# Performance work log

Measured on AMD Instinct MI355X. Metric: run time of the kernel, lower is better.

The kernel has to match this reference:

```python
import jax, jax.numpy as jnp
import numpy as np

T = 8192   # sequence length (= max_seq_len)
E = 1024   # embedding dim
D = 11     # hard-coded projection dim in source


def setup_inputs() -> dict:
    key = jax.random.key(0)
    ks = jax.random.split(key, 6)
    s_e = 1.0 / np.sqrt(E)
    s_d = 1.0 / np.sqrt(D)
    return {
        "x": jax.random.randint(ks[0], (T,), 0, 32000, dtype=jnp.int64),
        "x_embeddings": jax.random.normal(ks[1], (T, E), dtype=jnp.float32),
        "Wk": jax.random.normal(ks[2], (D, E), dtype=jnp.float32) * s_e,
        "bk": jnp.zeros((D,), dtype=jnp.float32),
        "Wq": jax.random.normal(ks[3], (D, E), dtype=jnp.float32) * s_e,
        "bq": jnp.zeros((D,), dtype=jnp.float32),
        "Wv": jax.random.normal(ks[4], (D, E), dtype=jnp.float32) * s_e,
        "bv": jnp.zeros((D,), dtype=jnp.float32),
        "Wf": jax.random.normal(ks[5], (E, D), dtype=jnp.float32) * s_d,
        "bf": jnp.zeros((E,), dtype=jnp.float32),
    }


def reference(x, x_embeddings, Wk, bk, Wq, bq, Wv, bv, Wf, bf):
    t = x.shape[0]  # static under jit
    k = x_embeddings @ Wk.T + bk            # [T, D]
    q = x_embeddings @ Wq.T + bq            # [T, D]
    v = x_embeddings @ Wv.T + bv            # [T, D]
    att = q @ k.T                           # [T, T]; NOTE: no 1/sqrt(D) scaling in source
    causal = jnp.tril(jnp.ones((t, t), dtype=bool))
    att = jnp.where(causal, att, -jnp.inf)
    att = jax.nn.softmax(att, axis=1)       # dim=1 as in source
    res = att @ v                           # [T, D]
    return res @ Wf.T + bf                  # [T, E]
```

## Files before the change

### kernel.cpp

```cpp
#include <hip/hip_runtime.h>

#define T_SEQ 8192
#define E_DIM 1024
#define QS 36
#define QNEC 4
#define QKC 64
#define QX4 16
#define QXST 17
#define QRB 64
#define AJC 64
#define ARB 256
#define KVW 24
#define NSLOT 128
#define TR 16

__device__ __forceinline__ float2 pkfma(float2 a, float2 b, float2 c) {
    return make_float2(fmaf(a.x, b.x, c.x), fmaf(a.y, b.y, c.y));
}
__device__ __forceinline__ float2 f2(float x, float y) { return make_float2(x, y); }


__global__ __launch_bounds__(256) void qkv_proj(
    const float* __restrict__ xe,
    const float* __restrict__ Wk, const float* __restrict__ bk,
    const float* __restrict__ Wq, const float* __restrict__ bq,
    const float* __restrict__ Wv, const float* __restrict__ bv,
    float* __restrict__ partQ) {
    const int row0 = blockIdx.x * QRB;
    const int ec = blockIdx.y;
    const int lane = threadIdx.x & 63;
    const int wg = threadIdx.x >> 6;

    __shared__ float4 xT[QRB * QXST];
    __shared__ float4 wT[36 * QX4];

    float2 acc[9];
#pragma unroll
    for (int k = 0; k < 9; ++k) acc[k] = f2(0.f, 0.f);

    for (int cc = 0; cc < 4; ++cc) {
        const int cb = ec * 256 + cc * QKC;
        if (cc) __syncthreads();

#pragma unroll
        for (int t = 0; t < 4; ++t) {
            int idx = threadIdx.x + t * 256;
            int r = idx >> 4, c4 = idx & 15;
            xT[r * QXST + c4] =
                *(const float4*)(xe + (size_t)(row0 + r) * E_DIM + cb + c4 * 4);
        }
        for (int idx = threadIdx.x; idx < 36 * QX4; idx += 256) {
            int r = idx >> 4, c4 = idx & 15;
            float4 v = make_float4(0.f, 0.f, 0.f, 0.f);
            if (r < 33) {
                const float* base = (r < 11) ? (Wk + (size_t)r * E_DIM)
                                  : (r < 22) ? (Wq + (size_t)(r - 11) * E_DIM)
                                             : (Wv + (size_t)(r - 22) * E_DIM);
                v = *(const float4*)(base + cb + c4 * 4);
            }
            wT[idx] = v;
        }
        __syncthreads();

        const float4* xr = xT + lane * QXST;
        const float4* wr = wT + wg * 9 * QX4;
#pragma unroll 4
        for (int c4 = 0; c4 < QX4; ++c4) {
            float4 xv = xr[c4];
#pragma unroll
            for (int k = 0; k < 9; ++k) {
                float4 wv = wr[k * QX4 + c4];
                acc[k] = pkfma(f2(xv.x, xv.y), f2(wv.x, wv.y), acc[k]);
                acc[k] = pkfma(f2(xv.z, xv.w), f2(wv.z, wv.w), acc[k]);
            }
        }
    }

    __syncthreads();
    float* res = (float*)xT;
#pragma unroll
    for (int k = 0; k < 9; ++k) {
        int o = wg * 9 + k;
        bool live = (o < 33);
        int c = (o < 11) ? o : (o < 22) ? o + 1 : (o < 33) ? o + 2
              : (o == 33) ? 11 : (o == 34) ? 23 : 35;
        float b = 0.f;
        if (ec == 0 && live)
            b = (o < 11) ? bk[o] : (o < 22) ? bq[o - 11] : bv[o - 22];
        res[lane * 36 + c] = live ? (acc[k].x + acc[k].y + b) : 0.f;
    }
    __syncthreads();

    float4* dst = (float4*)(partQ + ((size_t)ec * T_SEQ + row0) * QS);
    for (int idx = threadIdx.x; idx < QRB * 9; idx += 256) {
        int r = idx / 9, f = idx % 9;
        dst[idx] = *(const float4*)(res + r * 36 + f * 4);
    }
}

__global__ __launch_bounds__(256) void reduceQ(const float* __restrict__ partQ,
                                               float* __restrict__ qkvF) {
    const size_t idx = (size_t)blockIdx.x * 256 + threadIdx.x;
    const float4* p = (const float4*)partQ;
    const size_t cs = (size_t)T_SEQ * (QS / 4);
    float4 s = make_float4(0.f, 0.f, 0.f, 0.f);
#pragma unroll
    for (int c = 0; c < QNEC; ++c) {
        float4 a = p[idx + (size_t)c * cs];
        s.x += a.x; s.y += a.y; s.z += a.z; s.w += a.w;
    }
    ((float4*)qkvF)[idx] = s;
}

__global__ __launch_bounds__(128) void attn(const float* __restrict__ qkvF,
                                            float* __restrict__ part) {
    const int b = blockIdx.x;
    int rb = 0;
    while ((rb + 1) * (rb + 2) <= b) ++rb;
    const int p = b - rb * (rb + 1);
    const int lane = threadIdx.x & 63;
    const int wid = threadIdx.x >> 6;
    const int jc = 2 * p + wid;
    const int r0 = rb * ARB + lane * 4;
    const int j0 = jc * AJC;

    float2 q[4][6], o[4][6];
#pragma unroll
    for (int i = 0; i < 4; ++i) {
        const float* qp = qkvF + (size_t)(r0 + i) * QS + 12;
#pragma unroll
        for (int d = 0; d < 5; ++d) q[i][d] = f2(qp[2 * d], qp[2 * d + 1]);
        q[i][5] = f2(qp[10], 0.f);
#pragma unroll
        for (int d = 0; d < 6; ++d) o[i][d] = f2(0.f, 0.f);
    }

    __shared__ float kvs[2][AJC * KVW];
    float* kv = kvs[wid];

#pragma unroll
    for (int t = 0; t < 6; ++t) {
        int idx = lane + t * 64;
        int row = idx / 6, f = idx % 6;
        int srcOff = f * 4 + (f >= 3 ? 12 : 0);
        float4 v = *(const float4*)(qkvF + (size_t)(j0 + row) * QS + srcOff);
        *(float4*)(kv + row * KVW + f * 4) = v;
    }
    __syncthreads();

    for (int jj = 0; jj < AJC; ++jj) {
        const float* kp = kv + jj * KVW;
        const float4 kA = *(const float4*)(kp);
        const float4 kB = *(const float4*)(kp + 4);
        const float4 kC = *(const float4*)(kp + 8);
        const float4 vA = *(const float4*)(kp + 12);
        const float4 vB = *(const float4*)(kp + 16);
        const float4 vC = *(const float4*)(kp + 20);
        const float2 k01 = f2(kA.x, kA.y), k23 = f2(kA.z, kA.w);
        const float2 k45 = f2(kB.x, kB.y), k67 = f2(kB.z, kB.w);
        const float2 k89 = f2(kC.x, kC.y), kXp = f2(kC.z, kC.w);
        const int j = j0 + jj;

#pragma unroll
        for (int i = 0; i < 4; ++i) {
            float2 s = pkfma(q[i][0], k01, pkfma(q[i][1], k23, pkfma(q[i][2], k45,
                       pkfma(q[i][3], k67, pkfma(q[i][4], k89,
                       pkfma(q[i][5], kXp, f2(0.f, 0.f)))))));
            float pe = __expf(s.x + s.y);
            pe = (j <= r0 + i) ? pe : 0.f;
            float2 p2 = f2(pe, pe);
            o[i][0] = pkfma(p2, f2(vA.x, vA.y), o[i][0]);
            o[i][1] = pkfma(p2, f2(vA.z, vA.w), o[i][1]);
            o[i][2] = pkfma(p2, f2(vB.x, vB.y), o[i][2]);
            o[i][3] = pkfma(p2, f2(vB.z, vB.w), o[i][3]);
            o[i][4] = pkfma(p2, f2(vC.x, vC.y), o[i][4]);
            o[i][5] = pkfma(p2, f2(vC.z, 1.f),  o[i][5]);
        }
    }

    float* d0 = part + ((size_t)jc * T_SEQ + r0) * 12;
#pragma unroll
    for (int i = 0; i < 4; ++i) {
        float4 t;
        t.x = o[i][0].x; t.y = o[i][0].y; t.z = o[i][1].x; t.w = o[i][1].y;
        *(float4*)(d0 + i * 12 + 0) = t;
        t.x = o[i][2].x; t.y = o[i][2].y; t.z = o[i][3].x; t.w = o[i][3].y;
        *(float4*)(d0 + i * 12 + 4) = t;
        t.x = o[i][4].x; t.y = o[i][4].y; t.z = o[i][5].x; t.w = o[i][5].y;
        *(float4*)(d0 + i * 12 + 8) = t;
    }
}

__global__ __launch_bounds__(256) void pass2(const float* __restrict__ part,
                                             const float* __restrict__ Wf,
                                             const float* __restrict__ bf,
                                             float* __restrict__ out) {
    const int t0 = blockIdx.x * TR;
    const int cnt = 4 * (t0 / ARB) + 4;
    __shared__ float red[16][16][12];
    __shared__ float res[TR][12];
    {
        const int r = threadIdx.x >> 4;
        const int s = threadIdx.x & 15;
        float a[12];
#pragma unroll
        for (int d = 0; d < 12; ++d) a[d] = 0.f;
        const size_t S = (size_t)T_SEQ * 12;
        const float* p = part + (size_t)(t0 + r) * 12;
        for (int c = s; c < cnt; c += 16) {
            const float4* pc = (const float4*)(p + (size_t)c * S);
            float4 x0 = pc[0], x1 = pc[1], x2 = pc[2];
            a[0] += x0.x; a[1] += x0.y; a[2]  += x0.z; a[3]  += x0.w;
            a[4] += x1.x; a[5] += x1.y; a[6]  += x1.z; a[7]  += x1.w;
            a[8] += x2.x; a[9] += x2.y; a[10] += x2.z; a[11] += x2.w;
        }
#pragma unroll
        for (int d = 0; d < 12; ++d) red[r][s][d] = a[d];
    }
    __syncthreads();
    if (threadIdx.x < TR * 12) {
        const int r = threadIdx.x / 12, d = threadIdx.x % 12;
        float sum = 0.f;
#pragma unroll
        for (int s = 0; s < 16; ++s) sum += red[r][s][d];
        res[r][d] = (d == 11) ? (1.f / sum) : sum;
    }
    __syncthreads();

    const int e0 = threadIdx.x * 4;
    float w[4][11];
    const float* wp = Wf + (size_t)e0 * 11;
#pragma unroll
    for (int ee = 0; ee < 4; ++ee)
#pragma unroll
        for (int i = 0; i < 11; ++i) w[ee][i] = wp[ee * 11 + i];
    const float4 bv = *(const float4*)(bf + e0);

    for (int r = 0; r < TR; ++r) {
        float rr[12];
#pragma unroll
        for (int d = 0; d < 12; ++d) rr[d] = res[r][d];
        float2 a0 = f2(0.f, 0.f), a1 = a0, a2 = a0, a3 = a0;
#pragma unroll
        for (int d = 0; d < 10; d += 2) {
            float2 rv = f2(rr[d], rr[d + 1]);
            a0 = pkfma(rv, f2(w[0][d], w[0][d + 1]), a0);
            a1 = pkfma(rv, f2(w[1][d], w[1][d + 1]), a1);
            a2 = pkfma(rv, f2(w[2][d], w[2][d + 1]), a2);
            a3 = pkfma(rv, f2(w[3][d], w[3][d + 1]), a3);
        }
        const float rl = rr[11];
        float4 ov;
        ov.x = (a0.x + a0.y + rr[10] * w[0][10]) * rl + bv.x;
        ov.y = (a1.x + a1.y + rr[10] * w[1][10]) * rl + bv.y;
        ov.z = (a2.x + a2.y + rr[10] * w[2][10]) * rl + bv.z;
        ov.w = (a3.x + a3.y + rr[10] * w[3][10]) * rl + bv.w;
        *(float4*)(out + (size_t)(t0 + r) * E_DIM + e0) = ov;
    }
}

extern "C" void kernel_launch(void* const* d_in, const int* in_sizes, int n_in,
                              void* d_out, int out_size, void* d_ws, size_t ws_size,
                              hipStream_t stream) {
    const float* xe = (const float*)d_in[1];
    const float* Wk = (const float*)d_in[2];
    const float* bk = (const float*)d_in[3];
    const float* Wq = (const float*)d_in[4];
    const float* bq = (const float*)d_in[5];
    const float* Wv = (const float*)d_in[6];
    const float* bv = (const float*)d_in[7];
    const float* Wf = (const float*)d_in[8];
    const float* bf = (const float*)d_in[9];
    float* out = (float*)d_out;

    float* qkvF  = (float*)d_ws;
    float* partQ = qkvF + (size_t)T_SEQ * QS;
    float* part  = partQ;

    qkv_proj<<<dim3(T_SEQ / QRB, QNEC), 256, 0, stream>>>(xe, Wk, bk, Wq, bq, Wv, bv, partQ);
    reduceQ<<<(T_SEQ * QS / 4) / 256, 256, 0, stream>>>(partQ, qkvF);
    const int nrg = T_SEQ / ARB;
    attn<<<nrg * (nrg + 1), 128, 0, stream>>>(qkvF, part);
    pass2<<<T_SEQ / TR, 256, 0, stream>>>(part, Wf, bf, out);
}
```

Measured before the change: 179.6 us.

## Reduce attention partials in-block across four waves and split QKV projection finer

The attention kernel now uses 256-thread blocks, with four waves each covering 32 key columns of a 128-column chunk. The four partial outputs are combined through shared memory in a two-step tree, so each block writes a single partial. This halves the partial buffer traffic that pass2 has to sum. Separately, the QKV projection is split into 8 E-chunks instead of 4 to get more blocks, at the cost of more partial sums in reduceQ. The extra barriers and LDS reduction add overhead in each attention block.

```diff
diff --git a/kernel.cpp b/kernel.cpp
--- a/kernel.cpp
+++ b/kernel.cpp
@@ -3,21 +3,28 @@
 #define T_SEQ 8192
 #define E_DIM 1024
 #define QS 36
-#define QNEC 4
+#define QNEC 8
 #define QKC 64
 #define QX4 16
 #define QXST 17
 #define QRB 64
-#define AJC 64
+#define AJW 32
+#define ABJ 128
 #define ARB 256
 #define KVW 24
-#define NSLOT 128
 #define TR 16
 
 __device__ __forceinline__ float2 pkfma(float2 a, float2 b, float2 c) {
     return make_float2(fmaf(a.x, b.x, c.x), fmaf(a.y, b.y, c.y));
 }
 __device__ __forceinline__ float2 f2(float x, float y) { return make_float2(x, y); }
+
+__device__ __forceinline__ void pack3(const float2 o[6], float4* dst) {
+    float4 t;
+    t.x = o[0].x; t.y = o[0].y; t.z = o[1].x; t.w = o[1].y; dst[0] = t;
+    t.x = o[2].x; t.y = o[2].y; t.z = o[3].x; t.w = o[3].y; dst[1] = t;
+    t.x = o[4].x; t.y = o[4].y; t.z = o[5].x; t.w = o[5].y; dst[2] = t;
+}
 
 
 __global__ __launch_bounds__(256) void qkv_proj(
@@ -38,8 +45,8 @@
 #pragma unroll
     for (int k = 0; k < 9; ++k) acc[k] = f2(0.f, 0.f);
 
-    for (int cc = 0; cc < 4; ++cc) {
-        const int cb = ec * 256 + cc * QKC;
+    for (int cc = 0; cc < 2; ++cc) {
+        const int cb = ec * 128 + cc * QKC;
         if (cc) __syncthreads();
 
 #pragma unroll
@@ -112,17 +119,16 @@
     ((float4*)qkvF)[idx] = s;
 }
 
-__global__ __launch_bounds__(128) void attn(const float* __restrict__ qkvF,
+__global__ __launch_bounds__(256) void attn(const float* __restrict__ qkvF,
                                             float* __restrict__ part) {
     const int b = blockIdx.x;
     int rb = 0;
     while ((rb + 1) * (rb + 2) <= b) ++rb;
-    const int p = b - rb * (rb + 1);
+    const int c = b - rb * (rb + 1);
     const int lane = threadIdx.x & 63;
     const int wid = threadIdx.x >> 6;
-    const int jc = 2 * p + wid;
     const int r0 = rb * ARB + lane * 4;
-    const int j0 = jc * AJC;
+    const int j0 = c * ABJ + wid * AJW;
 
     float2 q[4][6], o[4][6];
 #pragma unroll
@@ -135,20 +141,20 @@
         for (int d = 0; d < 6; ++d) o[i][d] = f2(0.f, 0.f);
     }
 
-    __shared__ float kvs[2][AJC * KVW];
+    __shared__ float kvs[4][AJW * KVW];
+    __shared__ float4 red[2][64 * 12];
     float* kv = kvs[wid];
 
 #pragma unroll
-    for (int t = 0; t < 6; ++t) {
+    for (int t = 0; t < 3; ++t) {
         int idx = lane + t * 64;
         int row = idx / 6, f = idx % 6;
         int srcOff = f * 4 + (f >= 3 ? 12 : 0);
         float4 v = *(const float4*)(qkvF + (size_t)(j0 + row) * QS + srcOff);
         *(float4*)(kv + row * KVW + f * 4) = v;
     }
-    __syncthreads();
-
-    for (int jj = 0; jj < AJC; ++jj) {
+
+    for (int jj = 0; jj < AJW; ++jj) {
         const float* kp = kv + jj * KVW;
         const float4 kA = *(const float4*)(kp);
         const float4 kB = *(const float4*)(kp + 4);
@@ -178,16 +184,42 @@
         }
     }
 
-    float* d0 = part + ((size_t)jc * T_SEQ + r0) * 12;
-#pragma unroll
-    for (int i = 0; i < 4; ++i) {
-        float4 t;
-        t.x = o[i][0].x; t.y = o[i][0].y; t.z = o[i][1].x; t.w = o[i][1].y;
-        *(float4*)(d0 + i * 12 + 0) = t;
-        t.x = o[i][2].x; t.y = o[i][2].y; t.z = o[i][3].x; t.w = o[i][3].y;
-        *(float4*)(d0 + i * 12 + 4) = t;
-        t.x = o[i][4].x; t.y = o[i][4].y; t.z = o[i][5].x; t.w = o[i][5].y;
-        *(float4*)(d0 + i * 12 + 8) = t;
+    __syncthreads();
+    if (wid >= 2) {
+        float4* dst = red[wid - 2] + lane * 12;
+#pragma unroll
+        for (int i = 0; i < 4; ++i) pack3(o[i], dst + i * 3);
+    }
+    __syncthreads();
+    if (wid < 2) {
+        const float4* src = red[wid] + lane * 12;
+#pragma unroll
+        for (int i = 0; i < 4; ++i) {
+            float4 s0 = src[i * 3 + 0], s1 = src[i * 3 + 1], s2 = src[i * 3 + 2];
+            o[i][0].x += s0.x; o[i][0].y += s0.y; o[i][1].x += s0.z; o[i][1].y += s0.w;
+            o[i][2].x += s1.x; o[i][2].y += s1.y; o[i][3].x += s1.z; o[i][3].y += s1.w;
+            o[i][4].x += s2.x; o[i][4].y += s2.y; o[i][5].x += s2.z; o[i][5].y += s2.w;
+        }
+    }
+    __syncthreads();
+    if (wid == 1) {
+        float4* dst = red[0] + lane * 12;
+#pragma unroll
+        for (int i = 0; i < 4; ++i) pack3(o[i], dst + i * 3);
+    }
+    __syncthreads();
+    if (wid == 0) {
+        const float4* src = red[0] + lane * 12;
+#pragma unroll
+        for (int i = 0; i < 4; ++i) {
+            float4 s0 = src[i * 3 + 0], s1 = src[i * 3 + 1], s2 = src[i * 3 + 2];
+            o[i][0].x += s0.x; o[i][0].y += s0.y; o[i][1].x += s0.z; o[i][1].y += s0.w;
+            o[i][2].x += s1.x; o[i][2].y += s1.y; o[i][3].x += s1.z; o[i][3].y += s1.w;
+            o[i][4].x += s2.x; o[i][4].y += s2.y; o[i][5].x += s2.z; o[i][5].y += s2.w;
+        }
+        float* d0 = part + ((size_t)c * T_SEQ + r0) * 12;
+#pragma unroll
+        for (int i = 0; i < 4; ++i) pack3(o[i], (float4*)(d0 + i * 12));
     }
 }
 
@@ -196,7 +228,7 @@
                                              const float* __restrict__ bf,
                                              float* __restrict__ out) {
     const int t0 = blockIdx.x * TR;
-    const int cnt = 4 * (t0 / ARB) + 4;
+    const int cnt = 2 * (t0 / ARB) + 2;
     __shared__ float red[16][16][12];
     __shared__ float res[TR][12];
     {
@@ -280,6 +312,6 @@
     qkv_proj<<<dim3(T_SEQ / QRB, QNEC), 256, 0, stream>>>(xe, Wk, bk, Wq, bq, Wv, bv, partQ);
     reduceQ<<<(T_SEQ * QS / 4) / 256, 256, 0, stream>>>(partQ, qkvF);
     const int nrg = T_SEQ / ARB;
-    attn<<<nrg * (nrg + 1), 128, 0, stream>>>(qkvF, part);
+    attn<<<nrg * (nrg + 1), 256, 0, stream>>>(qkvF, part);
     pass2<<<T_SEQ / TR, 256, 0, stream>>>(part, Wf, bf, out);
 }
```

Measured after the change: 169.0 us. 5.9% less time.
